# Kernel optimization log

Hardware: AMD Instinct MI355X
Metric: run time of the kernel (lower is better)

## Reference

```python
import jax, jax.numpy as jnp
import numpy as np

T, B, V, E, HID, K = 1024, 128, 65536, 128, 256, 64
H = HID // 2  # per-direction LSTM hidden


def setup_inputs() -> dict:
    key = jax.random.key(0)
    ks = jax.random.split(key, 18)
    s = 0.05
    f32 = jnp.float32
    return {
        "kmers": jax.random.randint(ks[0], (T, B), 0, V),
        "tags": jax.random.randint(ks[1], (B,), 0, K),
        "emb": jax.random.normal(ks[2], (V, E), f32) * s,
        "w_ih_f": jax.random.normal(ks[3], (4 * H, E), f32) * s,
        "w_hh_f": jax.random.normal(ks[4], (4 * H, H), f32) * s,
        "b_ih_f": jax.random.normal(ks[5], (4 * H,), f32) * s,
        "b_hh_f": jax.random.normal(ks[6], (4 * H,), f32) * s,
        "w_ih_b": jax.random.normal(ks[7], (4 * H, E), f32) * s,
        "w_hh_b": jax.random.normal(ks[8], (4 * H, H), f32) * s,
        "b_ih_b": jax.random.normal(ks[9], (4 * H,), f32) * s,
        "b_hh_b": jax.random.normal(ks[10], (4 * H,), f32) * s,
        "w_proj": jax.random.normal(ks[11], (K, HID), f32) * s,
        "b_proj": jax.random.normal(ks[12], (K,), f32) * s,
        "start_trans": jax.random.uniform(ks[13], (K,), f32, -0.1, 0.1),
        "end_trans": jax.random.uniform(ks[14], (K,), f32, -0.1, 0.1),
        "trans": jax.random.uniform(ks[15], (K, K), f32, -0.1, 0.1),
    }


def _lstm_dir(x, w_ih, w_hh, b_ih, b_hh):
    # x: [T, B, E] -> hidden states [T, B, H]; PyTorch gate order i,f,g,o
    b = b_ih + b_hh
    xg = jnp.einsum('tbe,ge->tbg', x, w_ih) + b  # precompute input gates
    Bd = x.shape[1]
    Hd = w_hh.shape[1]
    def step(carry, g_in):
        h, c = carry
        g = g_in + h @ w_hh.T
        i, f, gg, o = jnp.split(g, 4, axis=-1)
        c = jax.nn.sigmoid(f) * c + jax.nn.sigmoid(i) * jnp.tanh(gg)
        h = jax.nn.sigmoid(o) * jnp.tanh(c)
        return (h, c), h
    init = (jnp.zeros((Bd, Hd), x.dtype), jnp.zeros((Bd, Hd), x.dtype))
    _, hs = jax.lax.scan(step, init, xg)
    return hs


def reference(kmers, tags, emb, w_ih_f, w_hh_f, b_ih_f, b_hh_f,
              w_ih_b, w_hh_b, b_ih_b, b_hh_b, w_proj, b_proj,
              start_trans, end_trans, trans):
    x = emb[kmers]  # [T, B, E]
    h_f = _lstm_dir(x, w_ih_f, w_hh_f, b_ih_f, b_hh_f)
    h_b = _lstm_dir(x[::-1], w_ih_b, w_hh_b, b_ih_b, b_hh_b)[::-1]
    out = jnp.concatenate([h_f, h_b], axis=-1)  # [T, B, HID]
    emissions = jnp.einsum('tbh,kh->tbk', out, w_proj) + b_proj  # [T, B, K]

    # tags repeated along time (original: tags.repeat(sent_size, 1))
    tags_seq = jnp.broadcast_to(tags[None, :], (emissions.shape[0], tags.shape[0]))

    # CRF numerator: score of given tag sequence (full mask)
    em_sel = jnp.take_along_axis(emissions, tags_seq[:, :, None], axis=2)[..., 0]  # [T, B]
    numerator = (start_trans[tags_seq[0]] + em_sel.sum(0)
                 + trans[tags_seq[:-1], tags_seq[1:]].sum(0)
                 + end_trans[tags_seq[-1]])  # [B]

    # CRF denominator: forward algorithm (log partition)
    def fwd_step(score, em_t):
        # score: [B, K] -> logsumexp over previous tag
        nxt = jax.nn.logsumexp(score[:, :, None] + trans[None, :, :] + em_t[:, None, :], axis=1)
        return nxt, None
    init = start_trans[None, :] + emissions[0]  # [B, K]
    final, _ = jax.lax.scan(fwd_step, init, emissions[1:])
    denominator = jax.nn.logsumexp(final + end_trans[None, :], axis=1)  # [B]

    # torchcrf default reduction='sum'; module returns negated llh
    return (denominator - numerator).sum()
```

## Files before the change

### kernel.cpp

```cpp
#include <hip/hip_runtime.h>
#include <hip/hip_bf16.h>

typedef _Float16 half8_t __attribute__((ext_vector_type(8)));
typedef _Float16 half4_t __attribute__((ext_vector_type(4)));
typedef _Float16 half2_t __attribute__((ext_vector_type(2)));
typedef float float4_t __attribute__((ext_vector_type(4)));
typedef unsigned int uint2_t __attribute__((ext_vector_type(2)));

#define TT 1024
#define BB 128
#define EE 128
#define HH 128
#define NTAG 64
#define ASTR 144

__device__ __forceinline__ float fast_exp(float x) {
  return __builtin_amdgcn_exp2f(x * 1.44269504088896f);
}
__device__ __forceinline__ void lds_barrier() {
  asm volatile("s_waitcnt lgkmcnt(0)\n\ts_barrier" ::: "memory");
}
__device__ __forceinline__ half2_t cvt_pk(float a, float b) {
  return __builtin_bit_cast(half2_t, __builtin_amdgcn_cvt_pkrtz(a, b));
}
__device__ __forceinline__ half2_t h2bc(float v) {
  _Float16 h = (_Float16)v;
  half2_t r; r[0] = h; r[1] = h;
  return r;
}
__device__ __forceinline__ float quad_max4(float v) {
  unsigned a = __builtin_bit_cast(unsigned, v);
  uint2_t r = __builtin_amdgcn_permlane32_swap(a, a, false, false);
  float m = fmaxf(__builtin_bit_cast(float, r[0]), __builtin_bit_cast(float, r[1]));
  unsigned b = __builtin_bit_cast(unsigned, m);
  uint2_t s = __builtin_amdgcn_permlane16_swap(b, b, false, false);
  return fmaxf(__builtin_bit_cast(float, s[0]), __builtin_bit_cast(float, s[1]));
}
__device__ __forceinline__ half2_t tanh6(half2_t x) {
  half2_t y = __builtin_elementwise_min(__builtin_elementwise_max(x, h2bc(-1.6f)), h2bc(1.6f));
  half2_t u = y * y;
  half2_t p = u * h2bc(0.04667f) + h2bc(-0.28507f);
  p = u * p + h2bc(1.0f);
  return y * p;
}
__device__ __forceinline__ half2_t sig6(half2_t x) {
  half2_t y = __builtin_elementwise_min(__builtin_elementwise_max(x, h2bc(-3.2f)), h2bc(3.2f));
  half2_t u = y * y;
  half2_t q = u * h2bc(0.00072921875f) + h2bc(-0.017816875f);
  q = u * q + h2bc(0.25f);
  return y * q + h2bc(0.5f);
}

__global__ __launch_bounds__(256) void init_kernel(float4_t* __restrict__ p) {
  p[blockIdx.x * 256 + threadIdx.x] = (float4_t){0.f, 0.f, 0.f, 0.f};
}

__global__ __launch_bounds__(256) void embed_kernel(const int* __restrict__ kmers,
                                                    const float* __restrict__ emb,
                                                    half4_t* __restrict__ x) {
  const int g = blockIdx.x * 256 + threadIdx.x;
  const int row = g >> 5, seg = g & 31;
  const int km = kmers[row];
  const float4_t v = ((const float4_t*)(emb + (size_t)km * EE))[seg];
  half4_t o;
  o[0] = (_Float16)v[0]; o[1] = (_Float16)v[1];
  o[2] = (_Float16)v[2]; o[3] = (_Float16)v[3];
  x[(size_t)row * 32 + seg] = o;
}

__global__ __launch_bounds__(512) void xg_kernel(
    const _Float16* __restrict__ x,
    const float* __restrict__ w_ih_f, const float* __restrict__ b_ih_f, const float* __restrict__ b_hh_f,
    const float* __restrict__ w_ih_b, const float* __restrict__ b_ih_b, const float* __restrict__ b_hh_b,
    _Float16* __restrict__ xgbuf, int s, int Tseg) {
  const int nt = Tseg >> 4;
  const int wg = blockIdx.x;
  const int dir = wg / (8 * nt);
  const int rem = wg - dir * 8 * nt;
  const int chunk = rem / nt;
  const int tb = rem - chunk * nt;
  const int tid = threadIdx.x;
  const int wave = tid >> 6, lane = tid & 63;
  const int n16 = lane & 15, quad = lane >> 4;

  const float* wih = dir ? w_ih_b : w_ih_f;
  const float* bih = dir ? b_ih_b : b_ih_f;
  const float* bhh = dir ? b_hh_b : b_hh_f;

  half8_t wf[4][4];
#pragma unroll
  for (int g = 0; g < 4; ++g) {
    const int row = g * HH + wave * 16 + n16;
#pragma unroll
    for (int kf = 0; kf < 4; ++kf) {
      const float* src = wih + row * EE + kf * 32 + quad * 8;
#pragma unroll
      for (int i = 0; i < 8; ++i) wf[g][kf][i] = (_Float16)src[i];
    }
  }
  float4_t bias4[4];
#pragma unroll
  for (int g = 0; g < 4; ++g) {
    const int row = g * HH + wave * 16 + quad * 4;
    const float4_t bi = *(const float4_t*)(bih + row);
    const float4_t bh = *(const float4_t*)(bhh + row);
    bias4[g] = bi + bh;
  }

  const int l0 = tb * 16;
  half8_t xb[4];
  {
    const int te = dir ? (TT - 1 - (s * Tseg + l0)) : (s * Tseg + l0);
#pragma unroll
    for (int kf = 0; kf < 4; ++kf)
      xb[kf] = *(const half8_t*)(x + ((size_t)te * BB + chunk * 16 + n16) * EE + kf * 32 + quad * 8);
  }
  for (int u = 0; u < 16; ++u) {
    const int l = l0 + u;
    half8_t xn[4] = {};
    if (u < 15) {
      const int tn = dir ? (TT - 1 - (s * Tseg + l + 1)) : (s * Tseg + l + 1);
#pragma unroll
      for (int kf = 0; kf < 4; ++kf)
        xn[kf] = *(const half8_t*)(x + ((size_t)tn * BB + chunk * 16 + n16) * EE + kf * 32 + quad * 8);
    }
    float4_t acc[4];
#pragma unroll
    for (int g = 0; g < 4; ++g) acc[g] = bias4[g];
#pragma unroll
    for (int kf = 0; kf < 4; ++kf)
#pragma unroll
      for (int g = 0; g < 4; ++g)
        acc[g] = __builtin_amdgcn_mfma_f32_16x16x32_f16(wf[g][kf], xb[kf], acc[g], 0, 0, 0);
    half8_t ho0, ho1;
#pragma unroll
    for (int r = 0; r < 4; ++r) {
      ho0[r] = (_Float16)acc[0][r];
      ho0[4 + r] = (_Float16)acc[1][r];
      ho1[r] = (_Float16)acc[2][r];
      ho1[4 + r] = (_Float16)acc[3][r];
    }
    _Float16* ob = xgbuf + (size_t)dir * Tseg * 65536 + (size_t)l * 65536 + chunk * 8192 +
                   wave * 1024 + lane * 16;
    *(half8_t*)ob = ho0;
    *(half8_t*)(ob + 8) = ho1;
#pragma unroll
    for (int kf = 0; kf < 4; ++kf) xb[kf] = xn[kf];
  }
}

__global__ __launch_bounds__(512, 2) void lstm_kernel(
    const _Float16* __restrict__ xgbuf,
    const float* __restrict__ w_hh_f, const float* __restrict__ w_hh_b,
    _Float16* __restrict__ h_cat, _Float16* __restrict__ h_state, float* __restrict__ c_state,
    int s, int Tseg) {
  __shared__ _Float16 A[2][16 * ASTR];
  const int wg = blockIdx.x;
  const int dir = wg >> 3, chunk = wg & 7;
  const int b0 = chunk * 16;
  const float* w_hh = dir ? w_hh_b : w_hh_f;
  const int tid = threadIdx.x;
  const int wave = tid >> 6, lane = tid & 63;
  const int n16 = lane & 15, quad = lane >> 4;

  half8_t wf[4][4];
#pragma unroll
  for (int g = 0; g < 4; ++g) {
    const int row = g * HH + wave * 16 + n16;
#pragma unroll
    for (int kf = 0; kf < 4; ++kf) {
      const float* src = w_hh + row * HH + kf * 32 + quad * 8;
#pragma unroll
      for (int i = 0; i < 8; ++i) wf[g][kf][i] = (_Float16)src[i];
    }
  }
  const int sidx = ((wg * 8 + wave) * 64 + lane) * 4;
  half4_t h4 = *(const half4_t*)(h_state + sidx);
  float4_t c4 = *(const float4_t*)(c_state + sidx);
  half2_t c2[2];
  c2[0] = cvt_pk(c4[0], c4[1]);
  c2[1] = cvt_pk(c4[2], c4[3]);
  *(half4_t*)(&A[0][n16 * ASTR + wave * 16 + quad * 4]) = h4;

  const _Float16* xgw =
      xgbuf + (size_t)dir * Tseg * 65536 + chunk * 8192 + wave * 1024 + (size_t)lane * 16;
  half4_t hlast = h4;
  const float4_t z4 = {0.f, 0.f, 0.f, 0.f};
  const int te0 = dir ? (TT - 1 - s * Tseg) : (s * Tseg);
  _Float16* gp_run =
      h_cat + ((size_t)te0 * BB + b0 + n16) * 256 + dir * HH + wave * 16 + quad * 4;
  const ptrdiff_t dstep = dir ? -(ptrdiff_t)32768 : (ptrdiff_t)32768;

  half8_t pf0[4], pf1[4];
#pragma unroll
  for (int j = 0; j < 4; ++j) {
    const _Float16* p = xgw + (size_t)j * 65536;
    pf0[j] = *(const half8_t*)p;
    pf1[j] = *(const half8_t*)(p + 8);
  }
  lds_barrier();

#define LSTM_STEP(AB, AN, X0, X1)                                                          \
  {                                                                                        \
    const _Float16* Abp = &AB[0];                                                          \
    _Float16* Anp = &AN[0];                                                                \
    half8_t hb0 = *(const half8_t*)(Abp + n16 * ASTR + 0 * 32 + quad * 8);                 \
    half8_t hb1 = *(const half8_t*)(Abp + n16 * ASTR + 1 * 32 + quad * 8);                 \
    half8_t hb2 = *(const half8_t*)(Abp + n16 * ASTR + 2 * 32 + quad * 8);                 \
    half8_t hb3 = *(const half8_t*)(Abp + n16 * ASTR + 3 * 32 + quad * 8);                 \
    float4_t acc[4];                                                                       \
    _Pragma("unroll") for (int g = 0; g < 4; ++g) {                                        \
      acc[g] = __builtin_amdgcn_mfma_f32_16x16x32_f16(wf[g][0], hb0, z4, 0, 0, 0);         \
    }                                                                                      \
    _Pragma("unroll") for (int g = 0; g < 4; ++g) {                                        \
      acc[g] = __builtin_amdgcn_mfma_f32_16x16x32_f16(wf[g][1], hb1, acc[g], 0, 0, 0);     \
    }                                                                                      \
    _Pragma("unroll") for (int g = 0; g < 4; ++g) {                                        \
      acc[g] = __builtin_amdgcn_mfma_f32_16x16x32_f16(wf[g][2], hb2, acc[g], 0, 0, 0);     \
    }                                                                                      \
    _Pragma("unroll") for (int g = 0; g < 4; ++g) {                                        \
      acc[g] = __builtin_amdgcn_mfma_f32_16x16x32_f16(wf[g][3], hb3, acc[g], 0, 0, 0);     \
    }                                                                                      \
    const half2_t* x0p = (const half2_t*)&X0;                                              \
    const half2_t* x1p = (const half2_t*)&X1;                                              \
    half4_t hstore;                                                                        \
    _Pragma("unroll") for (int p = 0; p < 2; ++p) {                                        \
      const half2_t i_ = sig6(cvt_pk(acc[0][2 * p], acc[0][2 * p + 1]) + x0p[p]);          \
      const half2_t f_ = sig6(cvt_pk(acc[1][2 * p], acc[1][2 * p + 1]) + x0p[2 + p]);      \
      const half2_t g_ = tanh6(cvt_pk(acc[2][2 * p], acc[2][2 * p + 1]) + x1p[p]);         \
      const half2_t o_ = sig6(cvt_pk(acc[3][2 * p], acc[3][2 * p + 1]) + x1p[2 + p]);      \
      c2[p] = f_ * c2[p] + i_ * g_;                                                        \
      const half2_t hh = o_ * tanh6(c2[p]);                                                \
      hstore[2 * p] = hh[0];                                                               \
      hstore[2 * p + 1] = hh[1];                                                           \
    }                                                                                      \
    *(half4_t*)(Anp + n16 * ASTR + wave * 16 + quad * 4) = hstore;                         \
    *(half4_t*)gp_run = hstore;                                                            \
    hlast = hstore;                                                                        \
  }

  for (int il = 0; il < Tseg; il += 4) {
#pragma unroll
    for (int j = 0; j < 4; ++j) {
      const half8_t xc0 = pf0[j], xc1 = pf1[j];
      int tf = il + j + 4;
      tf = tf >= Tseg ? Tseg - 1 : tf;
      const _Float16* p = xgw + (size_t)tf * 65536;
      pf0[j] = *(const half8_t*)p;
      pf1[j] = *(const half8_t*)(p + 8);
      lds_barrier();
      if (j & 1) {
        LSTM_STEP(A[1], A[0], xc0, xc1);
      } else {
        LSTM_STEP(A[0], A[1], xc0, xc1);
      }
      gp_run += dstep;
    }
  }
#undef LSTM_STEP

  *(half4_t*)(h_state + sidx) = hlast;
  c4[0] = (float)c2[0][0]; c4[1] = (float)c2[0][1];
  c4[2] = (float)c2[1][0]; c4[3] = (float)c2[1][1];
  *(float4_t*)(c_state + sidx) = c4;
}

__global__ __launch_bounds__(256) void emis_kernel(const _Float16* __restrict__ h_cat,
                                                   const float* __restrict__ w_proj,
                                                   const float* __restrict__ b_proj,
                                                   float* __restrict__ em,
                                                   _Float16* __restrict__ expem) {
  const int tid = threadIdx.x;
  const int wave = tid >> 6, lane = tid & 63;
  const int n16 = lane & 15, quad = lane >> 4;
  const size_t row0 = (size_t)blockIdx.x * 64 + wave * 16;

  half8_t bf[4][8];
#pragma unroll
  for (int nt = 0; nt < 4; ++nt) {
    const float* wp = w_proj + (nt * 16 + n16) * 256;
#pragma unroll
    for (int kf = 0; kf < 8; ++kf) {
      const int kb = kf * 32 + quad * 8;
#pragma unroll
      for (int i = 0; i < 8; ++i) bf[nt][kf][i] = (_Float16)wp[kb + i];
    }
  }
  float4_t acc[4];
#pragma unroll
  for (int nt = 0; nt < 4; ++nt) {
    const float bv = b_proj[nt * 16 + n16];
    acc[nt] = (float4_t){bv, bv, bv, bv};
  }
#pragma unroll
  for (int kf = 0; kf < 8; ++kf) {
    half8_t af = *(const half8_t*)(h_cat + (row0 + n16) * 256 + kf * 32 + quad * 8);
#pragma unroll
    for (int nt = 0; nt < 4; ++nt)
      acc[nt] = __builtin_amdgcn_mfma_f32_16x16x32_f16(af, bf[nt][kf], acc[nt], 0, 0, 0);
  }
#pragma unroll
  for (int nt = 0; nt < 4; ++nt)
#pragma unroll
    for (int r = 0; r < 4; ++r) {
      const size_t idx = (row0 + quad * 4 + r) * NTAG + nt * 16 + n16;
      em[idx] = acc[nt][r];
      expem[idx] = (_Float16)fast_exp(acc[nt][r]);
    }
}

__global__ __launch_bounds__(64) void crf_kernel(const float* __restrict__ em,
                                                 const _Float16* __restrict__ expem,
                                                 const float* __restrict__ trans,
                                                 const float* __restrict__ start_trans,
                                                 const float* __restrict__ end_trans,
                                                 _Float16* __restrict__ amid,
                                                 float* __restrict__ scmid) {
  const int lane = threadIdx.x;
  const int n16 = lane & 15, quad = lane >> 4;
  const int side = blockIdx.x >> 3;
  const int bg = blockIdx.x & 7;
  const int gb = bg * 16 + n16;

  half8_t efA[4][2];
#pragma unroll
  for (int mt = 0; mt < 4; ++mt)
#pragma unroll
    for (int kf = 0; kf < 2; ++kf)
#pragma unroll
      for (int i = 0; i < 8; ++i) {
        const int m = mt * 16 + n16, k = kf * 32 + quad * 8 + i;
        const float tv = side ? trans[m * NTAG + k] : trans[k * NTAG + m];
        efA[mt][kf][i] = (_Float16)(fast_exp(tv) * 0.015625f);
      }

  float sv[16];
#pragma unroll
  for (int kf = 0; kf < 2; ++kf) {
    const int j0 = kf * 32 + quad * 8;
#pragma unroll
    for (int i = 0; i < 8; ++i)
      sv[kf * 8 + i] =
          side ? end_trans[j0 + i] : (start_trans[j0 + i] + em[(size_t)gb * NTAG + j0 + i]);
  }
  float m0;
  {
    float mx[8];
#pragma unroll
    for (int i = 0; i < 8; ++i) mx[i] = fmaxf(sv[i], sv[8 + i]);
#pragma unroll
    for (int i = 0; i < 4; ++i) mx[i] = fmaxf(mx[i], mx[4 + i]);
    m0 = fmaxf(fmaxf(mx[0], mx[1]), fmaxf(mx[2], mx[3]));
    m0 = quad_max4(m0);
  }
  half8_t pb[2];
#pragma unroll
  for (int kf = 0; kf < 2; ++kf)
#pragma unroll
    for (int i = 0; i < 8; ++i) pb[kf][i] = (_Float16)fast_exp(sv[kf * 8 + i] - m0);
  float lz2 = 0.f;
  const float4_t z4 = {0.f, 0.f, 0.f, 0.f};
  const _Float16* exb = expem + (size_t)gb * NTAG;

#define CRF_CORE(PB0, PB1)                                                                 \
    float4_t a0 = __builtin_amdgcn_mfma_f32_16x16x32_f16(efA[0][0], PB0, z4, 0, 0, 0);     \
    float4_t a1 = __builtin_amdgcn_mfma_f32_16x16x32_f16(efA[1][0], PB0, z4, 0, 0, 0);     \
    float4_t a2 = __builtin_amdgcn_mfma_f32_16x16x32_f16(efA[2][0], PB0, z4, 0, 0, 0);     \
    float4_t a3 = __builtin_amdgcn_mfma_f32_16x16x32_f16(efA[3][0], PB0, z4, 0, 0, 0);     \
    a0 = __builtin_amdgcn_mfma_f32_16x16x32_f16(efA[0][1], PB1, a0, 0, 0, 0);              \
    a1 = __builtin_amdgcn_mfma_f32_16x16x32_f16(efA[1][1], PB1, a1, 0, 0, 0);              \
    a2 = __builtin_amdgcn_mfma_f32_16x16x32_f16(efA[2][1], PB1, a2, 0, 0, 0);              \
    a3 = __builtin_amdgcn_mfma_f32_16x16x32_f16(efA[3][1], PB1, a3, 0, 0, 0);              \
    half2_t dpk[4][2];                                                                     \
    dpk[0][0] = cvt_pk(a0[0], a0[1]); dpk[0][1] = cvt_pk(a0[2], a0[3]);                    \
    dpk[1][0] = cvt_pk(a1[0], a1[1]); dpk[1][1] = cvt_pk(a1[2], a1[3]);                    \
    dpk[2][0] = cvt_pk(a2[0], a2[1]); dpk[2][1] = cvt_pk(a2[2], a2[3]);                    \
    dpk[3][0] = cvt_pk(a3[0], a3[1]); dpk[3][1] = cvt_pk(a3[2], a3[3]);                    \
    half2_t ww[2][4];                                                                      \
    _Pragma("unroll") for (int kf = 0; kf < 2; ++kf)                                       \
      _Pragma("unroll") for (int p = 0; p < 2; ++p) {                                      \
        const unsigned Xu = __builtin_bit_cast(unsigned, dpk[2 * kf][p]);                  \
        const unsigned Yu = __builtin_bit_cast(unsigned, dpk[2 * kf + 1][p]);              \
        uint2_t r1 = __builtin_amdgcn_permlane32_swap(Xu, Yu, false, false);               \
        uint2_t r2 = __builtin_amdgcn_permlane16_swap(r1[0], r1[1], false, false);         \
        ww[kf][p] = __builtin_bit_cast(half2_t, r2[0]);                                    \
        ww[kf][2 + p] = __builtin_bit_cast(half2_t, r2[1]);                                \
      }

#define CRF_RESCALE(TCUR)                                                                  \
    if (((TCUR) & 15) == 0) {                                                              \
      half2_t* pw0 = (half2_t*)&pb[0];                                                     \
      half2_t* pw1 = (half2_t*)&pb[1];                                                     \
      half2_t m2 = __builtin_elementwise_max(pw0[0], pw0[1]);                              \
      m2 = __builtin_elementwise_max(m2, __builtin_elementwise_max(pw0[2], pw0[3]));       \
      m2 = __builtin_elementwise_max(m2, __builtin_elementwise_max(pw1[0], pw1[1]));       \
      m2 = __builtin_elementwise_max(m2, __builtin_elementwise_max(pw1[2], pw1[3]));       \
      float mm = fmaxf((float)m2[0], (float)m2[1]);                                        \
      mm = quad_max4(mm);                                                                  \
      lz2 += __builtin_amdgcn_logf(mm);                                                    \
      const half2_t rc = h2bc(__builtin_amdgcn_rcpf(mm));                                  \
      _Pragma("unroll") for (int j2 = 0; j2 < 4; ++j2) { pw0[j2] *= rc; pw1[j2] *= rc; }   \
    }

#define FWD_STEP(TCUR, GC0, GC1)                                                           \
  {                                                                                        \
    CRF_CORE(pb[0], pb[1])                                                                 \
    const half2_t* gw0 = (const half2_t*)&GC0;                                             \
    const half2_t* gw1 = (const half2_t*)&GC1;                                             \
    half2_t* pw0 = (half2_t*)&pb[0];                                                       \
    half2_t* pw1 = (half2_t*)&pb[1];                                                       \
    _Pragma("unroll") for (int w2 = 0; w2 < 4; ++w2) {                                     \
      pw0[w2] = ww[0][w2] * gw0[w2];                                                       \
      pw1[w2] = ww[1][w2] * gw1[w2];                                                       \
    }                                                                                      \
    CRF_RESCALE(TCUR)                                                                      \
  }

#define BWD_STEP(TCUR, GC0, GC1)                                                           \
  {                                                                                        \
    const half8_t pg0 = pb[0] * GC0;                                                       \
    const half8_t pg1 = pb[1] * GC1;                                                       \
    CRF_CORE(pg0, pg1)                                                                     \
    half2_t* pw0 = (half2_t*)&pb[0];                                                       \
    half2_t* pw1 = (half2_t*)&pb[1];                                                       \
    _Pragma("unroll") for (int w2 = 0; w2 < 4; ++w2) {                                     \
      pw0[w2] = ww[0][w2];                                                                 \
      pw1[w2] = ww[1][w2];                                                                 \
    }                                                                                      \
    CRF_RESCALE(TCUR)                                                                      \
  }

  half8_t pre0[8], pre1[8];
  if (side == 0) {
#pragma unroll
    for (int j = 0; j < 8; ++j) {
      pre0[j] = *(const half8_t*)(exb + (size_t)(1 + j) * 8192 + quad * 8);
      pre1[j] = *(const half8_t*)(exb + (size_t)(1 + j) * 8192 + 32 + quad * 8);
    }
    int t = 1;
    for (int grp = 0; grp < 64; ++grp) {
#pragma unroll
      for (int j = 0; j < 8; ++j) {
        const half8_t gc0 = pre0[j], gc1 = pre1[j];
        int tf = t + 8; tf = tf > 1023 ? 1023 : tf;
        pre0[j] = *(const half8_t*)(exb + (size_t)tf * 8192 + quad * 8);
        pre1[j] = *(const half8_t*)(exb + (size_t)tf * 8192 + 32 + quad * 8);
        FWD_STEP(t, gc0, gc1)
        ++t;
      }
    }
  } else {
#pragma unroll
    for (int j = 0; j < 8; ++j) {
      pre0[j] = *(const half8_t*)(exb + (size_t)(1023 - j) * 8192 + quad * 8);
      pre1[j] = *(const half8_t*)(exb + (size_t)(1023 - j) * 8192 + 32 + quad * 8);
    }
    int t = 1023;
    for (int grp = 0; grp < 63; ++grp) {
#pragma unroll
      for (int j = 0; j < 8; ++j) {
        const half8_t gc0 = pre0[j], gc1 = pre1[j];
        int tf = t - 8; tf = tf < 0 ? 0 : tf;
        pre0[j] = *(const half8_t*)(exb + (size_t)tf * 8192 + quad * 8);
        pre1[j] = *(const half8_t*)(exb + (size_t)tf * 8192 + 32 + quad * 8);
        BWD_STEP(t, gc0, gc1)
        --t;
      }
    }
    for (; t >= 513; --t) {
      const half8_t gc0 = *(const half8_t*)(exb + (size_t)t * 8192 + quad * 8);
      const half8_t gc1 = *(const half8_t*)(exb + (size_t)t * 8192 + 32 + quad * 8);
      BWD_STEP(t, gc0, gc1)
    }
  }
#undef FWD_STEP
#undef BWD_STEP
#undef CRF_RESCALE
#undef CRF_CORE

  _Float16* ap = amid + (size_t)(side * BB + gb) * NTAG;
  *(half8_t*)(ap + quad * 8) = pb[0];
  *(half8_t*)(ap + 32 + quad * 8) = pb[1];
  if (quad == 0)
    scmid[side * BB + gb] = m0 + 0.693147180559945f * lz2;
}

__global__ __launch_bounds__(256) void numer_kernel(const float* __restrict__ em,
                                                    const int* __restrict__ tags,
                                                    const float* __restrict__ trans,
                                                    const float* __restrict__ start_trans,
                                                    const float* __restrict__ end_trans,
                                                    float* __restrict__ num) {
  const int b = blockIdx.x;
  const int tg = tags[b];
  float acc = 0.f;
  for (int t = threadIdx.x; t < TT; t += 256)
    acc += em[((size_t)t * BB + b) * NTAG + tg];
#pragma unroll
  for (int off = 32; off > 0; off >>= 1) acc += __shfl_xor(acc, off, 64);
  __shared__ float red[4];
  if ((threadIdx.x & 63) == 0) red[threadIdx.x >> 6] = acc;
  __syncthreads();
  if (threadIdx.x == 0) {
    const float tot = red[0] + red[1] + red[2] + red[3];
    num[b] = start_trans[tg] + end_trans[tg] + 1023.0f * trans[tg * NTAG + tg] + tot;
  }
}

__global__ __launch_bounds__(128) void final_kernel(const _Float16* __restrict__ amid,
                                                    const float* __restrict__ scmid,
                                                    const float* __restrict__ num,
                                                    float* __restrict__ out) {
  const int b = threadIdx.x;
  const _Float16* af = amid + (size_t)b * NTAG;
  const _Float16* bf = amid + (size_t)(BB + b) * NTAG;
  float dot = 0.f;
#pragma unroll
  for (int kf = 0; kf < 8; ++kf) {
    const half8_t av = *(const half8_t*)(af + kf * 8);
    const half8_t bv = *(const half8_t*)(bf + kf * 8);
#pragma unroll
    for (int i = 0; i < 8; ++i) dot += (float)av[i] * (float)bv[i];
  }
  const float denomv = scmid[b] + scmid[BB + b] +
                       0.693147180559945f * (6138.0f + __builtin_amdgcn_logf(dot));
  float v = denomv - num[b];
#pragma unroll
  for (int off = 32; off > 0; off >>= 1) v += __shfl_xor(v, off, 64);
  __shared__ float red[2];
  if ((b & 63) == 0) red[b >> 6] = v;
  __syncthreads();
  if (b == 0) out[0] = red[0] + red[1];
}

extern "C" void kernel_launch(void* const* d_in, const int* in_sizes, int n_in,
                              void* d_out, int out_size, void* d_ws, size_t ws_size,
                              hipStream_t stream) {
  const int* kmers = (const int*)d_in[0];
  const int* tags = (const int*)d_in[1];
  const float* emb = (const float*)d_in[2];
  const float* w_ih_f = (const float*)d_in[3];
  const float* w_hh_f = (const float*)d_in[4];
  const float* b_ih_f = (const float*)d_in[5];
  const float* b_hh_f = (const float*)d_in[6];
  const float* w_ih_b = (const float*)d_in[7];
  const float* w_hh_b = (const float*)d_in[8];
  const float* b_ih_b = (const float*)d_in[9];
  const float* b_hh_b = (const float*)d_in[10];
  const float* w_proj = (const float*)d_in[11];
  const float* b_proj = (const float*)d_in[12];
  const float* start_trans = (const float*)d_in[13];
  const float* end_trans = (const float*)d_in[14];
  const float* trans = (const float*)d_in[15];

  int nseg;
  if (ws_size >= 235078656ull) nseg = 2;
  else if (ws_size >= 167969792ull) nseg = 4;
  else if (ws_size >= 134415360ull) nseg = 8;
  else nseg = 16;
  const int Tseg = TT / nseg;
  const size_t xg_bytes = 268435456ull / (size_t)nseg;

  char* ws = (char*)d_ws;
  half4_t* x = (half4_t*)ws;
  _Float16* h_cat = (_Float16*)(ws + 33554432);
  _Float16* xgbuf = (_Float16*)(ws + 100663296);
  _Float16* expem = (_Float16*)(ws + 100663296);
  _Float16* h_state = (_Float16*)(ws + 100663296 + xg_bytes);
  float* c_state = (float*)(ws + 100663296 + xg_bytes + 65536);
  _Float16* amid = (_Float16*)(ws + 100663296 + xg_bytes);
  float* scmid = (float*)(ws + 100663296 + xg_bytes + 32768);
  float* num = (float*)(ws + 100663296 + xg_bytes + 196608);
  float* em = (float*)ws;
  float* out = (float*)d_out;

  hipLaunchKernelGGL(init_kernel, dim3(48), dim3(256), 0, stream, (float4_t*)h_state);
  hipLaunchKernelGGL(embed_kernel, dim3(16384), dim3(256), 0, stream, kmers, emb, x);
  for (int s = 0; s < nseg; ++s) {
    hipLaunchKernelGGL(xg_kernel, dim3(Tseg), dim3(512), 0, stream, (const _Float16*)x,
                       w_ih_f, b_ih_f, b_hh_f, w_ih_b, b_ih_b, b_hh_b, xgbuf, s, Tseg);
    hipLaunchKernelGGL(lstm_kernel, dim3(16), dim3(512), 0, stream, (const _Float16*)xgbuf,
                       w_hh_f, w_hh_b, h_cat, h_state, c_state, s, Tseg);
  }
  hipLaunchKernelGGL(emis_kernel, dim3(2048), dim3(256), 0, stream, h_cat, w_proj, b_proj, em,
                     expem);
  hipLaunchKernelGGL(crf_kernel, dim3(16), dim3(64), 0, stream, em, (const _Float16*)expem,
                     trans, start_trans, end_trans, amid, scmid);
  hipLaunchKernelGGL(numer_kernel, dim3(128), dim3(256), 0, stream, em, tags, trans, start_trans,
                     end_trans, num);
  hipLaunchKernelGGL(final_kernel, dim3(1), dim3(128), 0, stream, amid, scmid, num, out);
}
```

Baseline: 1.015 ms.

## Overlap next segment's input-gate GEMM with LSTM recurrence via double-buffered fused launch

Merges the xg (input-gate projection) computation for segment s+1 into the same launch as the LSTM recurrence for segment s. Extra blocks beyond the first 16 compute the next segment's gates into a second buffer, so the 16 latency-bound recurrence blocks run alongside the GEMM instead of serially. It also reorders the step loop so the barrier and LSTM step come before the next xg prefetch, and peels the last four steps to drop the clamp. This uses twice the xg buffer memory and shares CUs between the GEMM blocks and the recurrence blocks, which could slow the critical recurrent path.

```diff
diff --git a/kernel.cpp b/kernel.cpp
--- a/kernel.cpp
+++ b/kernel.cpp
@@ -68,13 +68,12 @@
   x[(size_t)row * 32 + seg] = o;
 }
 
-__global__ __launch_bounds__(512) void xg_kernel(
-    const _Float16* __restrict__ x,
+__device__ __forceinline__ void xg_body(
+    int wg, const _Float16* __restrict__ x,
     const float* __restrict__ w_ih_f, const float* __restrict__ b_ih_f, const float* __restrict__ b_hh_f,
     const float* __restrict__ w_ih_b, const float* __restrict__ b_ih_b, const float* __restrict__ b_hh_b,
     _Float16* __restrict__ xgbuf, int s, int Tseg) {
   const int nt = Tseg >> 4;
-  const int wg = blockIdx.x;
   const int dir = wg / (8 * nt);
   const int rem = wg - dir * 8 * nt;
   const int chunk = rem / nt;
@@ -149,12 +148,27 @@
   }
 }
 
-__global__ __launch_bounds__(512, 2) void lstm_kernel(
-    const _Float16* __restrict__ xgbuf,
+__global__ __launch_bounds__(512) void xg_kernel(
+    const _Float16* __restrict__ x,
+    const float* __restrict__ w_ih_f, const float* __restrict__ b_ih_f, const float* __restrict__ b_hh_f,
+    const float* __restrict__ w_ih_b, const float* __restrict__ b_ih_b, const float* __restrict__ b_hh_b,
+    _Float16* __restrict__ xgbuf, int s, int Tseg) {
+  xg_body(blockIdx.x, x, w_ih_f, b_ih_f, b_hh_f, w_ih_b, b_ih_b, b_hh_b, xgbuf, s, Tseg);
+}
+
+__global__ __launch_bounds__(512, 2) void lstm_xg_kernel(
+    const _Float16* __restrict__ xgrd, _Float16* __restrict__ xgwr,
+    const _Float16* __restrict__ x,
     const float* __restrict__ w_hh_f, const float* __restrict__ w_hh_b,
+    const float* __restrict__ w_ih_f, const float* __restrict__ b_ih_f, const float* __restrict__ b_hh_f,
+    const float* __restrict__ w_ih_b, const float* __restrict__ b_ih_b, const float* __restrict__ b_hh_b,
     _Float16* __restrict__ h_cat, _Float16* __restrict__ h_state, float* __restrict__ c_state,
-    int s, int Tseg) {
+    int s, int sx, int Tseg) {
   __shared__ _Float16 A[2][16 * ASTR];
+  if (blockIdx.x >= 16) {
+    xg_body(blockIdx.x - 16, x, w_ih_f, b_ih_f, b_hh_f, w_ih_b, b_ih_b, b_hh_b, xgwr, sx, Tseg);
+    return;
+  }
   const int wg = blockIdx.x;
   const int dir = wg >> 3, chunk = wg & 7;
   const int b0 = chunk * 16;
@@ -183,7 +197,7 @@
   *(half4_t*)(&A[0][n16 * ASTR + wave * 16 + quad * 4]) = h4;
 
   const _Float16* xgw =
-      xgbuf + (size_t)dir * Tseg * 65536 + chunk * 8192 + wave * 1024 + (size_t)lane * 16;
+      xgrd + (size_t)dir * Tseg * 65536 + chunk * 8192 + wave * 1024 + (size_t)lane * 16;
   half4_t hlast = h4;
   const float4_t z4 = {0.f, 0.f, 0.f, 0.f};
   const int te0 = dir ? (TT - 1 - s * Tseg) : (s * Tseg);
@@ -198,7 +212,6 @@
     pf0[j] = *(const half8_t*)p;
     pf1[j] = *(const half8_t*)(p + 8);
   }
-  lds_barrier();
 
 #define LSTM_STEP(AB, AN, X0, X1)                                                          \
   {                                                                                        \
@@ -239,23 +252,30 @@
     hlast = hstore;                                                                        \
   }
 
-  for (int il = 0; il < Tseg; il += 4) {
+  for (int il = 0; il < Tseg - 4; il += 4) {
 #pragma unroll
     for (int j = 0; j < 4; ++j) {
-      const half8_t xc0 = pf0[j], xc1 = pf1[j];
-      int tf = il + j + 4;
-      tf = tf >= Tseg ? Tseg - 1 : tf;
-      const _Float16* p = xgw + (size_t)tf * 65536;
+      lds_barrier();
+      if (j & 1) {
+        LSTM_STEP(A[1], A[0], pf0[j], pf1[j]);
+      } else {
+        LSTM_STEP(A[0], A[1], pf0[j], pf1[j]);
+      }
+      const _Float16* p = xgw + (size_t)(il + j + 4) * 65536;
       pf0[j] = *(const half8_t*)p;
       pf1[j] = *(const half8_t*)(p + 8);
-      lds_barrier();
-      if (j & 1) {
-        LSTM_STEP(A[1], A[0], xc0, xc1);
-      } else {
-        LSTM_STEP(A[0], A[1], xc0, xc1);
-      }
       gp_run += dstep;
     }
+  }
+#pragma unroll
+  for (int j = 0; j < 4; ++j) {
+    lds_barrier();
+    if (j & 1) {
+      LSTM_STEP(A[1], A[0], pf0[j], pf1[j]);
+    } else {
+      LSTM_STEP(A[0], A[1], pf0[j], pf1[j]);
+    }
+    gp_run += dstep;
   }
 #undef LSTM_STEP
 
@@ -553,40 +573,78 @@
   const float* end_trans = (const float*)d_in[14];
   const float* trans = (const float*)d_in[15];
 
-  int nseg;
-  if (ws_size >= 235078656ull) nseg = 2;
-  else if (ws_size >= 167969792ull) nseg = 4;
-  else if (ws_size >= 134415360ull) nseg = 8;
-  else nseg = 16;
-  const int Tseg = TT / nseg;
-  const size_t xg_bytes = 268435456ull / (size_t)nseg;
-
   char* ws = (char*)d_ws;
   half4_t* x = (half4_t*)ws;
   _Float16* h_cat = (_Float16*)(ws + 33554432);
-  _Float16* xgbuf = (_Float16*)(ws + 100663296);
-  _Float16* expem = (_Float16*)(ws + 100663296);
-  _Float16* h_state = (_Float16*)(ws + 100663296 + xg_bytes);
-  float* c_state = (float*)(ws + 100663296 + xg_bytes + 65536);
-  _Float16* amid = (_Float16*)(ws + 100663296 + xg_bytes);
-  float* scmid = (float*)(ws + 100663296 + xg_bytes + 32768);
-  float* num = (float*)(ws + 100663296 + xg_bytes + 196608);
   float* em = (float*)ws;
   float* out = (float*)d_out;
 
-  hipLaunchKernelGGL(init_kernel, dim3(48), dim3(256), 0, stream, (float4_t*)h_state);
-  hipLaunchKernelGGL(embed_kernel, dim3(16384), dim3(256), 0, stream, kmers, emb, x);
-  for (int s = 0; s < nseg; ++s) {
+  const bool fused = ws_size >= 235078656ull;
+  if (fused) {
+    const int Tseg = 256;
+    _Float16* buf0 = (_Float16*)(ws + 100663296);
+    _Float16* buf1 = (_Float16*)(ws + 100663296 + 67108864);
+    _Float16* expem = (_Float16*)(ws + 100663296);
+    _Float16* h_state = (_Float16*)(ws + 100663296 + 134217728);
+    float* c_state = (float*)(ws + 100663296 + 134217728 + 65536);
+    _Float16* amid = (_Float16*)(ws + 100663296 + 134217728);
+    float* scmid = (float*)(ws + 100663296 + 134217728 + 32768);
+    float* num = (float*)(ws + 100663296 + 134217728 + 196608);
+
+    hipLaunchKernelGGL(init_kernel, dim3(48), dim3(256), 0, stream, (float4_t*)h_state);
+    hipLaunchKernelGGL(embed_kernel, dim3(16384), dim3(256), 0, stream, kmers, emb, x);
     hipLaunchKernelGGL(xg_kernel, dim3(Tseg), dim3(512), 0, stream, (const _Float16*)x,
-                       w_ih_f, b_ih_f, b_hh_f, w_ih_b, b_ih_b, b_hh_b, xgbuf, s, Tseg);
-    hipLaunchKernelGGL(lstm_kernel, dim3(16), dim3(512), 0, stream, (const _Float16*)xgbuf,
-                       w_hh_f, w_hh_b, h_cat, h_state, c_state, s, Tseg);
-  }
-  hipLaunchKernelGGL(emis_kernel, dim3(2048), dim3(256), 0, stream, h_cat, w_proj, b_proj, em,
-                     expem);
-  hipLaunchKernelGGL(crf_kernel, dim3(16), dim3(64), 0, stream, em, (const _Float16*)expem,
-                     trans, start_trans, end_trans, amid, scmid);
-  hipLaunchKernelGGL(numer_kernel, dim3(128), dim3(256), 0, stream, em, tags, trans, start_trans,
-                     end_trans, num);
-  hipLaunchKernelGGL(final_kernel, dim3(1), dim3(128), 0, stream, amid, scmid, num, out);
-}
+                       w_ih_f, b_ih_f, b_hh_f, w_ih_b, b_ih_b, b_hh_b, buf0, 0, Tseg);
+    for (int s = 0; s < 3; ++s) {
+      _Float16* rd = (s & 1) ? buf1 : buf0;
+      _Float16* wr = (s & 1) ? buf0 : buf1;
+      hipLaunchKernelGGL(lstm_xg_kernel, dim3(16 + Tseg), dim3(512), 0, stream,
+                         (const _Float16*)rd, wr, (const _Float16*)x, w_hh_f, w_hh_b,
+                         w_ih_f, b_ih_f, b_hh_f, w_ih_b, b_ih_b, b_hh_b,
+                         h_cat, h_state, c_state, s, s + 1, Tseg);
+    }
+    hipLaunchKernelGGL(lstm_xg_kernel, dim3(16), dim3(512), 0, stream,
+                       (const _Float16*)buf1, buf0, (const _Float16*)x, w_hh_f, w_hh_b,
+                       w_ih_f, b_ih_f, b_hh_f, w_ih_b, b_ih_b, b_hh_b,
+                       h_cat, h_state, c_state, 3, 0, Tseg);
+    hipLaunchKernelGGL(emis_kernel, dim3(2048), dim3(256), 0, stream, h_cat, w_proj, b_proj, em,
+                       expem);
+    hipLaunchKernelGGL(crf_kernel, dim3(16), dim3(64), 0, stream, em, (const _Float16*)expem,
+                       trans, start_trans, end_trans, amid, scmid);
+    hipLaunchKernelGGL(numer_kernel, dim3(128), dim3(256), 0, stream, em, tags, trans,
+                       start_trans, end_trans, num);
+    hipLaunchKernelGGL(final_kernel, dim3(1), dim3(128), 0, stream, amid, scmid, num, out);
+  } else {
+    int nseg;
+    if (ws_size >= 167969792ull) nseg = 4;
+    else if (ws_size >= 134415360ull) nseg = 8;
+    else nseg = 16;
+    const int Tseg = TT / nseg;
+    const size_t xg_bytes = 268435456ull / (size_t)nseg;
+    _Float16* xgbuf = (_Float16*)(ws + 100663296);
+    _Float16* expem = (_Float16*)(ws + 100663296);
+    _Float16* h_state = (_Float16*)(ws + 100663296 + xg_bytes);
+    float* c_state = (float*)(ws + 100663296 + xg_bytes + 65536);
+    _Float16* amid = (_Float16*)(ws + 100663296 + xg_bytes);
+    float* scmid = (float*)(ws + 100663296 + xg_bytes + 32768);
+    float* num = (float*)(ws + 100663296 + xg_bytes + 196608);
+
+    hipLaunchKernelGGL(init_kernel, dim3(48), dim3(256), 0, stream, (float4_t*)h_state);
+    hipLaunchKernelGGL(embed_kernel, dim3(16384), dim3(256), 0, stream, kmers, emb, x);
+    for (int s = 0; s < nseg; ++s) {
+      hipLaunchKernelGGL(xg_kernel, dim3(Tseg), dim3(512), 0, stream, (const _Float16*)x,
+                         w_ih_f, b_ih_f, b_hh_f, w_ih_b, b_ih_b, b_hh_b, xgbuf, s, Tseg);
+      hipLaunchKernelGGL(lstm_xg_kernel, dim3(16), dim3(512), 0, stream,
+                         (const _Float16*)xgbuf, xgbuf, (const _Float16*)x, w_hh_f, w_hh_b,
+                         w_ih_f, b_ih_f, b_hh_f, w_ih_b, b_ih_b, b_hh_b,
+                         h_cat, h_state, c_state, s, s, Tseg);
+    }
+    hipLaunchKernelGGL(emis_kernel, dim3(2048), dim3(256), 0, stream, h_cat, w_proj, b_proj, em,
+                       expem);
+    hipLaunchKernelGGL(crf_kernel, dim3(16), dim3(64), 0, stream, em, (const _Float16*)expem,
+                       trans, start_trans, end_trans, amid, scmid);
+    hipLaunchKernelGGL(numer_kernel, dim3(128), dim3(256), 0, stream, em, tags, trans,
+                       start_trans, end_trans, num);
+    hipLaunchKernelGGL(final_kernel, dim3(1), dim3(128), 0, stream, amid, scmid, num, out);
+  }
+}
```

After: 954.2 us. -6.0%, faster.
